# Kernel optimization log

Measured on AMD Instinct MI355X. Metric: run time of the kernel, lower is better.

## Reference

```python
import jax, jax.numpy as jnp
import numpy as np

B, S, D_MODEL, N_HEADS, D_K, D_V = 2, 2048, 1024, 16, 64, 64
LN_EPS = 1e-5


def setup_inputs() -> dict:
    key = jax.random.key(0)
    ks = jax.random.split(key, 10)
    scale = 1.0 / np.sqrt(D_MODEL)
    inp = {
        "input_Q": jax.random.normal(ks[0], (B, S, D_MODEL), jnp.float32),
        "input_K": jax.random.normal(ks[1], (B, S, D_MODEL), jnp.float32),
        "input_V": jax.random.normal(ks[2], (B, S, D_MODEL), jnp.float32),
        # causal mask (True = masked), as produced by attn_mask() with no pad tokens
        "attn_mask": jnp.broadcast_to(
            jnp.triu(jnp.ones((S, S), dtype=bool), k=1), (B, S, S)
        ),
        # weights stored [in, out] (equivalent to torch Linear weight.T)
        "W_Q": jax.random.normal(ks[3], (D_MODEL, N_HEADS * D_K), jnp.float32) * scale,
        "W_K": jax.random.normal(ks[4], (D_MODEL, N_HEADS * D_K), jnp.float32) * scale,
        "W_V": jax.random.normal(ks[5], (D_MODEL, N_HEADS * D_V), jnp.float32) * scale,
        "W_O": jax.random.normal(ks[6], (N_HEADS * D_V, D_MODEL), jnp.float32) * scale,
        "ln_gamma": jnp.ones((D_MODEL,), jnp.float32),
        "ln_beta": jnp.zeros((D_MODEL,), jnp.float32),
    }
    return inp


def _layernorm(x, gamma, beta):
    mu = jnp.mean(x, axis=-1, keepdims=True)
    var = jnp.var(x, axis=-1, keepdims=True)
    return (x - mu) * jax.lax.rsqrt(var + LN_EPS) * gamma + beta


def reference(input_Q, input_K, input_V, attn_mask, W_Q, W_K, W_V, W_O, ln_gamma, ln_beta):
    b = input_Q.shape[0]
    # projections -> [B, H, S, d]
    Q = (input_Q @ W_Q).reshape(b, -1, N_HEADS, D_K).transpose(0, 2, 1, 3)
    K = (input_K @ W_K).reshape(b, -1, N_HEADS, D_K).transpose(0, 2, 1, 3)
    V = (input_V @ W_V).reshape(b, -1, N_HEADS, D_V).transpose(0, 2, 1, 3)
    scores = jnp.einsum("bhqd,bhkd->bhqk", Q, K) / np.sqrt(D_K)
    scores = jnp.where(attn_mask[:, None, :, :], jnp.float32(-1e9), scores)
    attn = jax.nn.softmax(scores, axis=-1)
    context = jnp.einsum("bhqk,bhkd->bhqd", attn, V)
    context = context.transpose(0, 2, 1, 3).reshape(b, -1, N_HEADS * D_V)
    output = context @ W_O
    out = _layernorm(output + input_Q, ln_gamma, ln_beta)
    return out, attn
```

## Files before the change

kernel.cpp:

```cpp
#include <hip/hip_runtime.h>
#include <stdint.h>

typedef unsigned short u16;
typedef __attribute__((ext_vector_type(8))) short short8;
typedef __attribute__((ext_vector_type(4))) float f32x4;
typedef __attribute__((ext_vector_type(4))) unsigned short u16x4;
typedef __attribute__((ext_vector_type(4))) unsigned int uint4v;

#define MFMA16(a,b,c) __builtin_amdgcn_mfma_f32_16x16x32_bf16((a),(b),(c),0,0,0)
#define VWAIT(n) asm volatile("s_waitcnt vmcnt(" #n ")" ::: "memory")

__device__ __forceinline__ void gload16(const void* g, void* l) {
  __builtin_amdgcn_global_load_lds(
      (__attribute__((address_space(1))) void*)(uintptr_t)(g),
      (__attribute__((address_space(3))) void*)(uint32_t)(uintptr_t)(l),
      16, 0, 0);
}

__device__ __forceinline__ u16 f2bf(float x) {
  union { float f; unsigned u; } v; v.f = x;
  unsigned r = v.u + 0x7fffu + ((v.u >> 16) & 1u);
  return (u16)(r >> 16);
}
__device__ __forceinline__ unsigned pack2(float a, float b) {
  return (unsigned)f2bf(a) | ((unsigned)f2bf(b) << 16);
}

__global__ __launch_bounds__(256) void prep_kernel(const float* x0, const float* x1, const float* x2,
                                                   u16* y0, u16* y1, u16* y2,
                                                   const float* w0, const float* w1, const float* w2, const float* w3,
                                                   u16* t0, u16* t1, u16* t2, u16* t3) {
  __shared__ float tile[32][33];
  int z = blockIdx.y;
  if (z < 3) {
    const float* x = (z == 0) ? x0 : ((z == 1) ? x1 : x2);
    u16*         y = (z == 0) ? y0 : ((z == 1) ? y1 : y2);
    size_t i = ((size_t)blockIdx.x * 256 + threadIdx.x) * 4;
    float4 v = *(const float4*)(x + i);
    u16x4 o; o[0] = f2bf(v.x); o[1] = f2bf(v.y); o[2] = f2bf(v.z); o[3] = f2bf(v.w);
    *(u16x4*)(y + i) = o;
  } else {
    if (blockIdx.x >= 1024) return;
    const float* W; u16* T;
    switch (z - 3) {
      case 0:  W = w0; T = t0; break;
      case 1:  W = w1; T = t1; break;
      case 2:  W = w2; T = t2; break;
      default: W = w3; T = t3; break;
    }
    int k0 = (blockIdx.x >> 5) * 32, n0 = (blockIdx.x & 31) * 32;
    int tx = threadIdx.x & 31, ty = threadIdx.x >> 5;
#pragma unroll
    for (int j = 0; j < 4; ++j)
      tile[ty + 8*j][tx] = W[(size_t)(k0 + ty + 8*j) * 1024 + n0 + tx];
    __syncthreads();
#pragma unroll
    for (int j = 0; j < 4; ++j)
      T[(size_t)(n0 + ty + 8*j) * 1024 + k0 + tx] = f2bf(tile[tx][ty + 8*j]);
  }
}

__device__ __forceinline__ void gemm_stage(const u16* A, const u16* BT, int row0, int col0,
                                           int tid, int w, int kt, char* la, char* lb) {
#pragma unroll
  for (int j = 0; j < 2; ++j) {
    int c = j * 256 + tid;
    int mr = c & 127, kc = c >> 7;
    gload16(A  + (size_t)(row0 + mr) * 1024 + kt*32 + kc*8, la + (j*4 + w) * 1024);
    gload16(BT + (size_t)(col0 + mr) * 1024 + kt*32 + kc*8, lb + (j*4 + w) * 1024);
  }
}

__device__ __forceinline__ void gemm_core(const u16* A, const u16* BT, int row0, int col0,
                                          char* ldsA, char* ldsB, f32x4 (&acc)[4][4]) {
  int tid = threadIdx.x, w = tid >> 6, lane = tid & 63;
  int u = lane >> 4, c16 = lane & 15, wr = w >> 1, wc = w & 1;
  gemm_stage(A, BT, row0, col0, tid, w, 0, ldsA, ldsB);
  gemm_stage(A, BT, row0, col0, tid, w, 1, ldsA + 8192, ldsB + 8192);
  int cur = 0;
  for (int kt = 0; kt < 32; ++kt) {
    if (kt < 31) VWAIT(4);
    else         VWAIT(0);
    __builtin_amdgcn_s_barrier();
    asm volatile("" ::: "memory");
    if (kt < 30) {
      int nb = cur + 2; if (nb >= 3) nb -= 3;
      gemm_stage(A, BT, row0, col0, tid, w, kt + 2, ldsA + nb*8192, ldsB + nb*8192);
    }
    __builtin_amdgcn_sched_barrier(0);
    const char* la = ldsA + cur * 8192;
    const char* lb = ldsB + cur * 8192;
    short8 af[4], bv[4];
#pragma unroll
    for (int i = 0; i < 4; ++i) {
      af[i] = *(const short8*)(la + (u*128 + wr*64 + i*16 + c16) * 16);
      bv[i] = *(const short8*)(lb + (u*128 + wc*64 + i*16 + c16) * 16);
    }
#pragma unroll
    for (int i = 0; i < 4; ++i)
#pragma unroll
      for (int n = 0; n < 4; ++n)
        acc[i][n] = MFMA16(af[i], bv[n], acc[i][n]);
    cur = cur + 1; if (cur >= 3) cur = 0;
  }
}

__global__ __launch_bounds__(256) void gemm_qkv(const u16* Xq, const u16* Xk, const u16* Xv,
                                                const u16* WTq, const u16* WTk, const u16* WTv,
                                                u16* Qh, u16* Kh, u16* VhT) {
  __shared__ char ldsA[24576], ldsB[24576];
  int z = blockIdx.z;
  const u16* A  = (z == 0) ? Xq  : ((z == 1) ? Xk  : Xv);
  const u16* BT = (z == 0) ? WTq : ((z == 1) ? WTk : WTv);
  int id = blockIdx.x + 32 * blockIdx.y;
  int xcd = id & 7, rank = id >> 3;
  int row0 = (xcd * 4 + (rank & 3)) * 128;
  int col0 = (rank >> 2) * 128;
  f32x4 acc[4][4] = {};
  gemm_core(A, BT, row0, col0, ldsA, ldsB, acc);
  int tid = threadIdx.x, w = tid >> 6, lane = tid & 63, u = lane >> 4, c16 = lane & 15;
  int wr = w >> 1, wc = w & 1;
  if (z == 2) {
#pragma unroll
    for (int i = 0; i < 4; ++i)
#pragma unroll
      for (int n = 0; n < 4; ++n) {
        int rowb = row0 + wr*64 + i*16 + u*4;
        int colg = col0 + wc*64 + n*16 + c16;
        int b = rowb >> 11, s = rowb & 2047;
        int h = colg >> 6, d = colg & 63;
        u16x4 pv;
#pragma unroll
        for (int r = 0; r < 4; ++r) pv[r] = f2bf(acc[i][n][r]);
        *(u16x4*)(VhT + ((size_t)(b*16 + h) * 64 + d) * 2048 + s) = pv;
      }
  } else {
#pragma unroll
    for (int i = 0; i < 4; ++i)
#pragma unroll
      for (int n = 0; n < 4; ++n)
#pragma unroll
        for (int r = 0; r < 4; ++r) {
          int row = row0 + wr*64 + i*16 + u*4 + r;
          int colg = col0 + wc*64 + n*16 + c16;
          int b = row >> 11, s = row & 2047;
          int h = colg >> 6, d = colg & 63;
          float v = acc[i][n][r];
          if (z == 0) Qh[((size_t)(b*16 + h) * 2048 + s) * 64 + d] = f2bf(v * 0.125f);
          else        Kh[((size_t)(b*16 + h) * 2048 + s) * 64 + d] = f2bf(v);
        }
  }
}

__global__ __launch_bounds__(256) void gemm_out(const u16* Ctx, const u16* WTo,
                                                const float* resid, float* outF) {
  __shared__ char ldsA[24576], ldsB[24576];
  int id = blockIdx.x + 32 * blockIdx.y;
  int xcd = id & 7, rank = id >> 3;
  int row0 = (xcd * 4 + (rank & 3)) * 128;
  int col0 = (rank >> 2) * 128;
  f32x4 acc[4][4] = {};
  gemm_core(Ctx, WTo, row0, col0, ldsA, ldsB, acc);
  int tid = threadIdx.x, w = tid >> 6, lane = tid & 63, u = lane >> 4, c16 = lane & 15;
  int wr = w >> 1, wc = w & 1;
#pragma unroll
  for (int i = 0; i < 4; ++i)
#pragma unroll
    for (int n = 0; n < 4; ++n)
#pragma unroll
      for (int r = 0; r < 4; ++r) {
        int row = row0 + wr*64 + i*16 + u*4 + r;
        int colg = col0 + wc*64 + n*16 + c16;
        size_t idx = (size_t)row * 1024 + colg;
        outF[idx] = acc[i][n][r] + resid[idx];
      }
}

__device__ __forceinline__ void qk_tile(const char* Kbuf, short8 qf0, short8 qf1,
                                        int cq, int u, int rho, f32x4 (&acc)[4]) {
#pragma unroll
  for (int st = 0; st < 4; ++st) {
    short8 a0 = *(const short8*)(Kbuf + (st*16 + cq) * 128 + ((u*16) ^ rho));
    short8 a1 = *(const short8*)(Kbuf + (st*16 + cq) * 128 + ((64 + u*16) ^ rho));
    acc[st] = MFMA16(a0, qf0, acc[st]);
    acc[st] = MFMA16(a1, qf1, acc[st]);
  }
}

__device__ __forceinline__ void stage_k64(const u16* pan, int kt, char* buf, int tid, int w) {
#pragma unroll
  for (int j = 0; j < 2; ++j) {
    int c = j * 256 + tid;
    int row = c >> 3;
    int cc = (c & 7) ^ (row & 7);
    gload16(pan + (size_t)(kt*64 + row) * 64 + cc*8, buf + (j*4 + w) * 1024);
  }
}
__device__ __forceinline__ void stage_v64(const u16* vpan, int kt, char* buf, int tid, int w) {
#pragma unroll
  for (int j = 0; j < 2; ++j) {
    int c = j * 256 + tid;
    int d = c >> 3;
    int cc = (c & 7) ^ (d & 7);
    gload16(vpan + (size_t)d * 2048 + kt*64 + cc*8, buf + (j*4 + w) * 1024);
  }
}

__device__ __forceinline__ void tile_pass1(const char* Kcur, short8 qf0, short8 qf1,
                                           int q, int q0t, int kt, int ktd_t,
                                           int cq, int u, int rho, float& ls) {
  f32x4 acc[4] = {};
  qk_tile(Kcur, qf0, qf1, cq, u, rho, acc);
  if (kt == ktd_t) {
#pragma unroll
    for (int st = 0; st < 4; ++st)
#pragma unroll
      for (int r = 0; r < 4; ++r) {
        int key = q0t + st*16 + u*4 + r;
        if (key > q) acc[st][r] = -1e30f;
      }
  }
#pragma unroll
  for (int st = 0; st < 4; ++st)
#pragma unroll
    for (int r = 0; r < 4; ++r) ls += __expf(acc[st][r]);
}

__device__ __forceinline__ void tile_pass2(const char* Kcur, const char* Vcur, float* Pw,
                                           short8 qf0, short8 qf1, int q, int q0t, int kt, int ktd_t,
                                           float rl, float* apan, int w, int u, int cq,
                                           int rho, int sw, f32x4 (&ctx)[4]) {
  f32x4 acc[4] = {};
  __builtin_amdgcn_s_setprio(1);
  qk_tile(Kcur, qf0, qf1, cq, u, rho, acc);
  if (kt == ktd_t) {
#pragma unroll
    for (int st = 0; st < 4; ++st)
#pragma unroll
      for (int r = 0; r < 4; ++r) {
        int key = q0t + st*16 + u*4 + r;
        if (key > q) acc[st][r] = -1e30f;
      }
  }
#pragma unroll
  for (int st = 0; st < 4; ++st) {
    f32x4 p;
#pragma unroll
    for (int r = 0; r < 4; ++r) p[r] = __expf(acc[st][r]) * rl;
    *(f32x4*)&Pw[(cq*64 + st*16 + u*4) ^ sw] = p;
  }
  __builtin_amdgcn_sched_barrier(0);
#pragma unroll
  for (int j = 0; j < 4; ++j) {
    int row = j*4 + u;
    f32x4 v = *(const f32x4*)&Pw[(row*64 + cq*4) ^ ((row & 7) << 2)];
    __builtin_nontemporal_store(v,
        (f32x4*)(apan + (size_t)(q0t + w*16 + row) * 2048 + kt*64 + cq*4));
  }
#pragma unroll
  for (int wd = 0; wd < 2; ++wd) {
    int b0 = (cq*64 + wd*32 + u*8) ^ sw;
    f32x4 pa0 = *(const f32x4*)&Pw[b0];
    f32x4 pa1 = *(const f32x4*)&Pw[b0 ^ 4];
    uint4v pk;
    pk[0] = pack2(pa0[0], pa0[1]);
    pk[1] = pack2(pa0[2], pa0[3]);
    pk[2] = pack2(pa1[0], pa1[1]);
    pk[3] = pack2(pa1[2], pa1[3]);
    union { uint4v u4; short8 s8; } cvt; cvt.u4 = pk;
    short8 pa = cvt.s8;
#pragma unroll
    for (int nt = 0; nt < 4; ++nt) {
      short8 vb = *(const short8*)(Vcur + (nt*16 + cq) * 128 + ((wd*64 + u*16) ^ rho));
      ctx[nt] = MFMA16(pa, vb, ctx[nt]);
    }
  }
  __builtin_amdgcn_s_setprio(0);
  __builtin_amdgcn_sched_barrier(0);
}

__global__ __launch_bounds__(256) void attn_fused(const u16* Qh, const u16* Kh, const u16* VhT,
                                                  float* attnO, u16* Ctx) {
  __shared__ char Kl[3][8192];
  __shared__ char Vl[2][8192];
  __shared__ float Pf[4][1024];
  int tid = threadIdx.x, w = tid >> 6, lane = tid & 63;
  int u = lane >> 4, cq = lane & 15;
  int id = blockIdx.x;
  int xcd = id & 7, rank = id >> 3;
  int bh = xcd * 4 + (rank >> 4);
  int pi = rank & 15;
  int tlo = pi, thi = 31 - pi;
  int q0lo = tlo * 64, q0hi = thi * 64;
  int qlo = q0lo + w*16 + cq;
  int qhi = q0hi + w*16 + cq;
  int rho = (cq & 7) << 4;
  int sw  = (cq & 7) << 2;
  const u16* Kpan = Kh  + (size_t)bh * (2048 * 64);
  const u16* Vpan = VhT + (size_t)bh * (64 * 2048);
  const u16* Qlo = Qh + ((size_t)bh * 2048 + qlo) * 64;
  const u16* Qhi = Qh + ((size_t)bh * 2048 + qhi) * 64;
  short8 qlo0 = *(const short8*)(Qlo + u*8);
  short8 qlo1 = *(const short8*)(Qlo + 32 + u*8);
  short8 qhi0 = *(const short8*)(Qhi + u*8);
  short8 qhi1 = *(const short8*)(Qhi + 32 + u*8);

  float ls_lo = 0.f, ls_hi = 0.f;
  stage_k64(Kpan, 0, Kl[0], tid, w);
  stage_k64(Kpan, 1, Kl[1], tid, w);
  int cur1 = 0;
  for (int kt = 0; kt <= thi; ++kt) {
    if (kt < thi) VWAIT(4);
    else          VWAIT(0);
    __builtin_amdgcn_s_barrier();
    asm volatile("" ::: "memory");
    if (kt + 2 <= thi) {
      int nb = cur1 + 2; if (nb >= 3) nb -= 3;
      stage_k64(Kpan, kt + 2, Kl[nb], tid, w);
    }
    __builtin_amdgcn_sched_barrier(0);
    __builtin_amdgcn_s_setprio(1);
    tile_pass1(Kl[cur1], qhi0, qhi1, qhi, q0hi, kt, thi, cq, u, rho, ls_hi);
    if (kt <= tlo)
      tile_pass1(Kl[cur1], qlo0, qlo1, qlo, q0lo, kt, tlo, cq, u, rho, ls_lo);
    __builtin_amdgcn_s_setprio(0);
    cur1 = cur1 + 1; if (cur1 >= 3) cur1 = 0;
  }
  ls_lo += __shfl_xor(ls_lo, 16);  ls_lo += __shfl_xor(ls_lo, 32);
  ls_hi += __shfl_xor(ls_hi, 16);  ls_hi += __shfl_xor(ls_hi, 32);
  float rl_lo = 1.f / ls_lo, rl_hi = 1.f / ls_hi;

  asm volatile("" ::: "memory");
  __builtin_amdgcn_s_barrier();
  asm volatile("" ::: "memory");

  f32x4 ctx_lo[4] = {}, ctx_hi[4] = {};
  float* apan = attnO + (size_t)bh * 2048 * 2048;
  float* Pw = Pf[w];
  stage_k64(Kpan, 0, Kl[0], tid, w);
  stage_v64(Vpan, 0, Vl[0], tid, w);
  VWAIT(0);
  __builtin_amdgcn_s_barrier();
  asm volatile("" ::: "memory");
  for (int kt = 0; kt <= thi; ++kt) {
    int cur = kt & 1;
    if (kt < thi) {
      stage_k64(Kpan, kt + 1, Kl[cur ^ 1], tid, w);
      stage_v64(Vpan, kt + 1, Vl[cur ^ 1], tid, w);
    }
    __builtin_amdgcn_sched_barrier(0);
    tile_pass2(Kl[cur], Vl[cur], Pw, qhi0, qhi1, qhi, q0hi, kt, thi,
               rl_hi, apan, w, u, cq, rho, sw, ctx_hi);
    bool lo_act = (kt <= tlo);
    if (lo_act)
      tile_pass2(Kl[cur], Vl[cur], Pw, qlo0, qlo1, qlo, q0lo, kt, tlo,
                 rl_lo, apan, w, u, cq, rho, sw, ctx_lo);
    if (kt < thi) {
      if (lo_act) VWAIT(8);
      else        VWAIT(4);
      __builtin_amdgcn_s_barrier();
      asm volatile("" ::: "memory");
    }
  }

  f32x4 z4 = {};
  for (int kt = tlo + 1; kt < 32; ++kt)
#pragma unroll
    for (int j = 0; j < 4; ++j)
      __builtin_nontemporal_store(z4,
          (f32x4*)(apan + (size_t)(q0lo + w*16 + j*4 + u) * 2048 + kt*64 + cq*4));
  for (int kt = thi + 1; kt < 32; ++kt)
#pragma unroll
    for (int j = 0; j < 4; ++j)
      __builtin_nontemporal_store(z4,
          (f32x4*)(apan + (size_t)(q0hi + w*16 + j*4 + u) * 2048 + kt*64 + cq*4));

  int b = bh >> 4, h = bh & 15;
#pragma unroll
  for (int nt = 0; nt < 4; ++nt)
#pragma unroll
    for (int r = 0; r < 4; ++r) {
      int qr = q0lo + w*16 + u*4 + r;
      Ctx[((size_t)b * 2048 + qr) * 1024 + h*64 + nt*16 + cq] = f2bf(ctx_lo[nt][r]);
    }
#pragma unroll
  for (int nt = 0; nt < 4; ++nt)
#pragma unroll
    for (int r = 0; r < 4; ++r) {
      int qr = q0hi + w*16 + u*4 + r;
      Ctx[((size_t)b * 2048 + qr) * 1024 + h*64 + nt*16 + cq] = f2bf(ctx_hi[nt][r]);
    }
}

__global__ __launch_bounds__(256) void ln_kernel(const float* X, const float* g, const float* b, float* out) {
  int row = blockIdx.x, tid = threadIdx.x;
  float4 v = *(const float4*)(X + (size_t)row * 1024 + tid * 4);
  float s  = v.x + v.y + v.z + v.w;
  float q2 = v.x*v.x + v.y*v.y + v.z*v.z + v.w*v.w;
#pragma unroll
  for (int off = 32; off; off >>= 1) { s += __shfl_xor(s, off); q2 += __shfl_xor(q2, off); }
  __shared__ float red[8];
  int w = tid >> 6, lane = tid & 63;
  if (lane == 0) { red[w] = s; red[4 + w] = q2; }
  __syncthreads();
  s  = red[0] + red[1] + red[2] + red[3];
  q2 = red[4] + red[5] + red[6] + red[7];
  float mean = s * (1.f / 1024.f);
  float var  = q2 * (1.f / 1024.f) - mean * mean;
  float rs   = rsqrtf(var + 1e-5f);
  float4 gv = *(const float4*)(g + tid * 4);
  float4 bv = *(const float4*)(b + tid * 4);
  float4 o;
  o.x = (v.x - mean) * rs * gv.x + bv.x;
  o.y = (v.y - mean) * rs * gv.y + bv.y;
  o.z = (v.z - mean) * rs * gv.z + bv.z;
  o.w = (v.w - mean) * rs * gv.w + bv.w;
  *(float4*)(out + (size_t)row * 1024 + tid * 4) = o;
}

extern "C" void kernel_launch(void* const* d_in, const int* in_sizes, int n_in,
                              void* d_out, int out_size, void* d_ws, size_t ws_size,
                              hipStream_t stream) {
  (void)in_sizes; (void)n_in; (void)out_size; (void)ws_size;
  const float* inQ = (const float*)d_in[0];
  const float* inK = (const float*)d_in[1];
  const float* inV = (const float*)d_in[2];
  const float* Wq  = (const float*)d_in[4];
  const float* Wk  = (const float*)d_in[5];
  const float* Wv  = (const float*)d_in[6];
  const float* Wo  = (const float*)d_in[7];
  const float* gam = (const float*)d_in[8];
  const float* bet = (const float*)d_in[9];
  float* out   = (float*)d_out;
  float* attnO = out + (size_t)4194304;

  char* ws = (char*)d_ws;
  u16*   WTo    = (u16*)ws;
  u16*   Qh     = (u16*)(ws + 2097152);
  u16*   Kh     = (u16*)(ws + 2097152 + (size_t)8388608);
  u16*   VhT    = (u16*)(ws + 2097152 + (size_t)2*8388608);
  u16*   Ctx    = (u16*)(ws + 2097152 + (size_t)3*8388608);
  float* OutLin = (float*)(ws + 2097152 + (size_t)4*8388608);

  u16* Xbq = (u16*)attnO;
  u16* Xbk = Xbq + (size_t)4194304;
  u16* Xbv = Xbk + (size_t)4194304;
  u16* WTq = Xbv + (size_t)4194304;
  u16* WTk = WTq + (size_t)1048576;
  u16* WTv = WTk + (size_t)1048576;

  prep_kernel<<<dim3(4096, 7), 256, 0, stream>>>(inQ, inK, inV, Xbq, Xbk, Xbv,
                                                 Wq, Wk, Wv, Wo, WTq, WTk, WTv, WTo);
  gemm_qkv<<<dim3(32, 8, 3), 256, 0, stream>>>(Xbq, Xbk, Xbv, WTq, WTk, WTv, Qh, Kh, VhT);
  attn_fused<<<512, 256, 0, stream>>>(Qh, Kh, VhT, attnO, Ctx);
  gemm_out<<<dim3(32, 8), 256, 0, stream>>>(Ctx, WTo, inQ, OutLin);
  ln_kernel<<<4096, 256, 0, stream>>>(OutLin, gam, bet, out);
}
```

Before: 254.9 us.

## Overlap masked attention-zero stores with QKV GEMM main loop

Moves the zero-fill of the fully masked upper-triangle attention-probability tiles, for heads 3 and up, out of the attention kernel. The fill now runs as nontemporal stores spread across the k-loop iterations of the QKV projection GEMM, with vmcnt waits adjusted to account for the extra outstanding stores. Heads 0-2 are still zeroed in the attention kernel, because that region of the attention output buffer holds the bf16 input and weight scratch during the GEMM. The aim is to hide a large write-bandwidth cost behind MFMA compute. The risk is that the extra stores compete with the GEMM's own global loads and slow its pipeline.

```diff
diff --git a/kernel.cpp b/kernel.cpp
--- a/kernel.cpp
+++ b/kernel.cpp
@@ -71,16 +71,27 @@
   }
 }
 
+template <int ZF>
 __device__ __forceinline__ void gemm_core(const u16* A, const u16* BT, int row0, int col0,
-                                          char* ldsA, char* ldsB, f32x4 (&acc)[4][4]) {
+                                          char* ldsA, char* ldsB, f32x4 (&acc)[4][4],
+                                          int zbase, float* zdst) {
   int tid = threadIdx.x, w = tid >> 6, lane = tid & 63;
   int u = lane >> 4, c16 = lane & 15, wr = w >> 1, wc = w & 1;
   gemm_stage(A, BT, row0, col0, tid, w, 0, ldsA, ldsB);
   gemm_stage(A, BT, row0, col0, tid, w, 1, ldsA + 8192, ldsB + 8192);
   int cur = 0;
   for (int kt = 0; kt < 32; ++kt) {
-    if (kt < 31) VWAIT(4);
-    else         VWAIT(0);
+    if (ZF) {
+      if (kt == 0)       VWAIT(4);
+      else if (kt == 1)  VWAIT(7);
+      else if (kt <= 26) VWAIT(10);
+      else if (kt == 27) VWAIT(7);
+      else if (kt < 31)  VWAIT(4);
+      else               VWAIT(0);
+    } else {
+      if (kt < 31) VWAIT(4);
+      else         VWAIT(0);
+    }
     __builtin_amdgcn_s_barrier();
     asm volatile("" ::: "memory");
     if (kt < 30) {
@@ -88,6 +99,28 @@
       gemm_stage(A, BT, row0, col0, tid, w, kt + 2, ldsA + nb*8192, ldsB + nb*8192);
     }
     __builtin_amdgcn_sched_barrier(0);
+    if (ZF && kt < 26) {
+      f32x4 z4 = {};
+#pragma unroll
+      for (int s = 0; s < 3; ++s) {
+        int si = kt * 3 + s;
+        int pp = zbase + (si >> 1);
+        if (pp > 29695) pp = 29695;
+        int half = si & 1;
+        int bh = 3 + (pp >> 10);
+        int rp = pp & 1023;
+        int qt1 = rp >> 6;
+        int len1 = 496 - (qt1 << 4);
+        int slot = (half << 8) + tid;
+        if (slot > 495) slot = 495;
+        int row, col4;
+        if (slot < len1) { row = rp;        col4 = (qt1 << 4) + 16 + slot; }
+        else             { row = 2047 - rp; col4 = slot + 16; }
+        __builtin_nontemporal_store(z4,
+            (f32x4*)(zdst + ((size_t)bh * 2048 + row) * 2048 + (size_t)col4 * 4));
+      }
+      __builtin_amdgcn_sched_barrier(0);
+    }
     const char* la = ldsA + cur * 8192;
     const char* lb = ldsB + cur * 8192;
     short8 af[4], bv[4];
@@ -107,7 +140,7 @@
 
 __global__ __launch_bounds__(256) void gemm_qkv(const u16* Xq, const u16* Xk, const u16* Xv,
                                                 const u16* WTq, const u16* WTk, const u16* WTv,
-                                                u16* Qh, u16* Kh, u16* VhT) {
+                                                u16* Qh, u16* Kh, u16* VhT, float* attnO) {
   __shared__ char ldsA[24576], ldsB[24576];
   int z = blockIdx.z;
   const u16* A  = (z == 0) ? Xq  : ((z == 1) ? Xk  : Xv);
@@ -116,8 +149,10 @@
   int xcd = id & 7, rank = id >> 3;
   int row0 = (xcd * 4 + (rank & 3)) * 128;
   int col0 = (rank >> 2) * 128;
+  int id768 = blockIdx.x + 32 * blockIdx.y + 256 * z;
+  int zbase = id768 * 39;
   f32x4 acc[4][4] = {};
-  gemm_core(A, BT, row0, col0, ldsA, ldsB, acc);
+  gemm_core<1>(A, BT, row0, col0, ldsA, ldsB, acc, zbase, attnO);
   int tid = threadIdx.x, w = tid >> 6, lane = tid & 63, u = lane >> 4, c16 = lane & 15;
   int wr = w >> 1, wc = w & 1;
   if (z == 2) {
@@ -160,7 +195,7 @@
   int row0 = (xcd * 4 + (rank & 3)) * 128;
   int col0 = (rank >> 2) * 128;
   f32x4 acc[4][4] = {};
-  gemm_core(Ctx, WTo, row0, col0, ldsA, ldsB, acc);
+  gemm_core<0>(Ctx, WTo, row0, col0, ldsA, ldsB, acc, 0, nullptr);
   int tid = threadIdx.x, w = tid >> 6, lane = tid & 63, u = lane >> 4, c16 = lane & 15;
   int wr = w >> 1, wc = w & 1;
 #pragma unroll
@@ -363,17 +398,19 @@
     }
   }
 
-  f32x4 z4 = {};
-  for (int kt = tlo + 1; kt < 32; ++kt)
-#pragma unroll
-    for (int j = 0; j < 4; ++j)
-      __builtin_nontemporal_store(z4,
-          (f32x4*)(apan + (size_t)(q0lo + w*16 + j*4 + u) * 2048 + kt*64 + cq*4));
-  for (int kt = thi + 1; kt < 32; ++kt)
-#pragma unroll
-    for (int j = 0; j < 4; ++j)
-      __builtin_nontemporal_store(z4,
-          (f32x4*)(apan + (size_t)(q0hi + w*16 + j*4 + u) * 2048 + kt*64 + cq*4));
+  if (bh < 3) {
+    f32x4 z4 = {};
+    for (int kt = tlo + 1; kt < 32; ++kt)
+#pragma unroll
+      for (int j = 0; j < 4; ++j)
+        __builtin_nontemporal_store(z4,
+            (f32x4*)(apan + (size_t)(q0lo + w*16 + j*4 + u) * 2048 + kt*64 + cq*4));
+    for (int kt = thi + 1; kt < 32; ++kt)
+#pragma unroll
+      for (int j = 0; j < 4; ++j)
+        __builtin_nontemporal_store(z4,
+            (f32x4*)(apan + (size_t)(q0hi + w*16 + j*4 + u) * 2048 + kt*64 + cq*4));
+  }
 
   int b = bh >> 4, h = bh & 15;
 #pragma unroll
@@ -451,7 +488,7 @@
 
   prep_kernel<<<dim3(4096, 7), 256, 0, stream>>>(inQ, inK, inV, Xbq, Xbk, Xbv,
                                                  Wq, Wk, Wv, Wo, WTq, WTk, WTv, WTo);
-  gemm_qkv<<<dim3(32, 8, 3), 256, 0, stream>>>(Xbq, Xbk, Xbv, WTq, WTk, WTv, Qh, Kh, VhT);
+  gemm_qkv<<<dim3(32, 8, 3), 256, 0, stream>>>(Xbq, Xbk, Xbv, WTq, WTk, WTv, Qh, Kh, VhT, attnO);
   attn_fused<<<512, 256, 0, stream>>>(Qh, Kh, VhT, attnO, Ctx);
   gemm_out<<<dim3(32, 8), 256, 0, stream>>>(Ctx, WTo, inQ, OutLin);
   ln_kernel<<<4096, 256, 0, stream>>>(OutLin, gam, bet, out);
```

After: 232.2 us. 1.1x faster.
